# Performance work log

Measured on AMD Instinct MI355X. Metric: run time of the kernel, lower is better.

Reference implementation:

```python
import jax, jax.numpy as jnp
import numpy as np

HEADS = 8
DIM_HEAD = 64
LN_EPS = 1e-5


def rotate_half(x):
    # pairs (x0,x1) -> (-x1,x0), interleaved layout (einops '(d r)' with r=2)
    x1 = x[..., 0::2]
    x2 = x[..., 1::2]
    return jnp.stack((-x2, x1), axis=-1).reshape(x.shape)


def apply_rope(freqs, x):
    return x * jnp.cos(freqs) + rotate_half(x) * jnp.sin(freqs)


def setup_inputs() -> dict:
    key = jax.random.key(0)
    ks = jax.random.split(key, 4)
    b, n, dim = 2, 4096, 512
    inner = HEADS * DIM_HEAD
    x = jax.random.normal(ks[0], (b, n, dim), dtype=jnp.float32)
    rotary_time_emb = jax.random.uniform(ks[1], (b, n, DIM_HEAD), jnp.float32, 0.0, 6.283185)
    ln_w = jnp.ones((dim,), jnp.float32)
    ln_b = jnp.zeros((dim,), jnp.float32)
    w_qkv = jax.random.normal(ks[2], (inner * 3, dim), jnp.float32) * (dim ** -0.5)
    w_out = jax.random.normal(ks[3], (dim, inner), jnp.float32) * (inner ** -0.5)
    b_out = jnp.zeros((dim,), jnp.float32)
    return dict(x=x, rotary_time_emb=rotary_time_emb, ln_w=ln_w, ln_b=ln_b,
                w_qkv=w_qkv, w_out=w_out, b_out=b_out)


def reference(x, rotary_time_emb, ln_w, ln_b, w_qkv, w_out, b_out):
    b, n, dim = x.shape
    # LayerNorm
    mu = jnp.mean(x, axis=-1, keepdims=True)
    var = jnp.var(x, axis=-1, keepdims=True)
    xn = (x - mu) * jax.lax.rsqrt(var + LN_EPS) * ln_w + ln_b
    # QKV projection (Linear, no bias)
    qkv = xn @ w_qkv.T  # [b, n, 3*inner]
    q, k, v = jnp.split(qkv, 3, axis=-1)

    def to_heads(t):
        return t.reshape(b, n, HEADS, DIM_HEAD).transpose(0, 2, 1, 3)  # b h n d

    q, k, v = to_heads(q), to_heads(k), to_heads(v)
    freqs = rotary_time_emb[:, None, :, :]  # b 1 n d, broadcast over heads
    q = apply_rope(freqs, q)
    k = apply_rope(freqs, k)
    v = apply_rope(freqs, v)  # rotate_value=True
    scale = jnp.asarray(DIM_HEAD ** -0.5, dtype=x.dtype)
    scores = jnp.einsum('bhqd,bhkd->bhqk', q, k) * scale
    attn = jax.nn.softmax(scores, axis=-1)
    out = jnp.einsum('bhqk,bhkd->bhqd', attn, v)
    out = apply_rope(-freqs, out)  # inverse rotation of the output
    out = out.transpose(0, 2, 1, 3).reshape(b, n, HEADS * DIM_HEAD)
    return out @ w_out.T + b_out
```

## Files before the change

### kernel.cpp

```cpp
#include <hip/hip_runtime.h>
#include <cmath>

typedef short bf16x8 __attribute__((ext_vector_type(8)));
typedef float f32x2 __attribute__((ext_vector_type(2)));
typedef float f32x4 __attribute__((ext_vector_type(4)));
typedef float f32x16 __attribute__((ext_vector_type(16)));

#define NSEQ 4096
#define BATCH 2
#define DIM 512
#define HEADS 8
#define NROWS (BATCH * NSEQ)
#define QKVN (3 * DIM)

__device__ __forceinline__ unsigned short f2bf(float f) {
  unsigned int u = __float_as_uint(f);
  u += 0x7fffu + ((u >> 16) & 1u);
  return (unsigned short)(u >> 16);
}
__device__ __forceinline__ float bf2f(unsigned short h) {
  return __uint_as_float(((unsigned int)h) << 16);
}
__device__ __forceinline__ void gload16(const unsigned short* g, unsigned short* l) {
  __builtin_amdgcn_global_load_lds((const __attribute__((address_space(1))) unsigned int*)g,
                                   (__attribute__((address_space(3))) unsigned int*)l, 16, 0, 0);
}

__global__ __launch_bounds__(256) void k_prep(const float* __restrict__ rot,
                                              float* __restrict__ cosT,
                                              float* __restrict__ sinT,
                                              const float* __restrict__ wqkv,
                                              unsigned short* __restrict__ wqkb,
                                              const float* __restrict__ wout,
                                              unsigned short* __restrict__ wob,
                                              const float* __restrict__ x,
                                              const float* __restrict__ lnw,
                                              const float* __restrict__ lnb,
                                              unsigned short* __restrict__ xn) {
  const float INV2PI = 0.15915494309f;
  int bid = blockIdx.x;
  int t = threadIdx.x;
  if (bid < 2048) {
    int i = bid * 256 + t;
    float rv = rot[i] * INV2PI;
    cosT[i] = __builtin_amdgcn_cosf(rv);
    sinT[i] = __builtin_amdgcn_sinf(rv);
  } else if (bid < 5120) {
    int i = (bid - 2048) * 256 + t;
    wqkb[i] = f2bf(wqkv[i]);
  } else if (bid < 6144) {
    int i = (bid - 5120) * 256 + t;
    wob[i] = f2bf(wout[i]);
  } else {
    int row = (bid - 6144) * 4 + (t >> 6);
    int lane = t & 63;
    const float* xr = x + (size_t)row * DIM;
    float v[8];
    float s = 0.f;
#pragma unroll
    for (int j = 0; j < 8; ++j) { v[j] = xr[lane + j * 64]; s += v[j]; }
#pragma unroll
    for (int m = 1; m < 64; m <<= 1) s += __shfl_xor(s, m);
    float mu = s * (1.0f / DIM);
    float q = 0.f;
#pragma unroll
    for (int j = 0; j < 8; ++j) { float d = v[j] - mu; q += d * d; }
#pragma unroll
    for (int m = 1; m < 64; m <<= 1) q += __shfl_xor(q, m);
    float rs = rsqrtf(q * (1.0f / DIM) + 1e-5f);
#pragma unroll
    for (int j = 0; j < 8; ++j) {
      int col = lane + j * 64;
      xn[(size_t)row * DIM + col] = f2bf((v[j] - mu) * rs * lnw[col] + lnb[col]);
    }
  }
}

template <int EPI, int TM>
__global__ __launch_bounds__(256) void k_gemm(const unsigned short* __restrict__ A,
                                              const unsigned short* __restrict__ B,
                                              void* __restrict__ C,
                                              const float* __restrict__ bias,
                                              int M, int N, int K) {
  constexpr int MI = TM / 32;
  __shared__ __align__(16) unsigned short As[3][TM * 32];
  __shared__ __align__(16) unsigned short Bs[3][128 * 32];
  int bm = blockIdx.x, bn = blockIdx.y;
  int tid = threadIdx.x;
  int lane = tid & 63, w = tid >> 6;
  int wm = (w >> 1) * (TM / 2), wn = (w & 1) << 6;
  f32x4 acc[MI][4] = {};

#define GSTAGE(KT, BUF) do { \
  if constexpr (TM == 128) { \
    _Pragma("unroll") \
    for (int i = 0; i < 2; ++i) { \
      int c = tid + (i << 8); \
      int row = c >> 2, kc = (c & 3) << 3; \
      gload16(A + (size_t)(bm * 128 + row) * K + (KT) + kc, &As[BUF][(w * 64 + i * 256) * 8]); \
    } \
  } else { \
    int row = tid >> 2, kc = (tid & 3) << 3; \
    gload16(A + (size_t)(bm * 64 + row) * K + (KT) + kc, &As[BUF][(w * 64) * 8]); \
  } \
  _Pragma("unroll") \
  for (int i = 0; i < 2; ++i) { \
    int c = tid + (i << 8); \
    int row = c >> 2, kc = (c & 3) << 3; \
    gload16(B + (size_t)(bn * 128 + row) * K + (KT) + kc, &Bs[BUF][(w * 64 + i * 256) * 8]); \
  } } while (0)

  GSTAGE(0, 0);
  int nk = K >> 5;
  int rbuf = 0, wbuf = 1;
  for (int t = 0; t < nk; ++t) {
    if (t + 1 < nk) {
      GSTAGE((t + 1) << 5, wbuf);
      if constexpr (TM == 128) {
        asm volatile("s_waitcnt vmcnt(4)" ::: "memory");
      } else {
        asm volatile("s_waitcnt vmcnt(3)" ::: "memory");
      }
    } else {
      asm volatile("s_waitcnt vmcnt(0)" ::: "memory");
    }
    __builtin_amdgcn_s_barrier();
    asm volatile("" ::: "memory");
    bf16x8 af[MI], bfr[4];
#pragma unroll
    for (int mi = 0; mi < MI; ++mi)
      af[mi] = *(const bf16x8*)&As[rbuf][(wm + mi * 16 + (lane & 15)) * 32 + ((lane >> 4) << 3)];
#pragma unroll
    for (int ni = 0; ni < 4; ++ni)
      bfr[ni] = *(const bf16x8*)&Bs[rbuf][(wn + ni * 16 + (lane & 15)) * 32 + ((lane >> 4) << 3)];
#pragma unroll
    for (int mi = 0; mi < MI; ++mi)
#pragma unroll
      for (int ni = 0; ni < 4; ++ni)
        acc[mi][ni] = __builtin_amdgcn_mfma_f32_16x16x32_bf16(af[mi], bfr[ni], acc[mi][ni], 0, 0, 0);
    rbuf = (rbuf == 2) ? 0 : rbuf + 1;
    wbuf = (wbuf == 2) ? 0 : wbuf + 1;
  }
#undef GSTAGE
#pragma unroll
  for (int mi = 0; mi < MI; ++mi) {
#pragma unroll
    for (int ni = 0; ni < 4; ++ni) {
#pragma unroll
      for (int r = 0; r < 4; ++r) {
        int gm = bm * TM + wm + mi * 16 + ((lane >> 4) << 2) + r;
        int gn = bn * 128 + wn + ni * 16 + (lane & 15);
        if (EPI == 0) {
          ((unsigned short*)C)[(size_t)gm * N + gn] = f2bf(acc[mi][ni][r]);
        } else {
          ((float*)C)[(size_t)gm * N + gn] = acc[mi][ni][r] + bias[gn];
        }
      }
    }
  }
}

__global__ __launch_bounds__(256) void k_rope_split(const unsigned short* __restrict__ qkv,
                                                    const float* __restrict__ cosT,
                                                    const float* __restrict__ sinT,
                                                    unsigned short* __restrict__ qh,
                                                    unsigned short* __restrict__ kh,
                                                    unsigned short* __restrict__ vt) {
  __shared__ unsigned short vs[128][65];
  const float QSC = 0.125f * 1.44269504f;
  int nt = blockIdx.x, bh = blockIdx.y;
  int b = bh >> 3, h = bh & 7;
  int n0 = nt * 128;
  int t = threadIdx.x;
  int sub = t >> 3, cc = t & 7;
#pragma unroll
  for (int rr = 0; rr < 4; ++rr) {
    int row = rr * 32 + sub;
    int n = n0 + row;
    size_t base = ((size_t)(b * NSEQ + n)) * QKVN + h * 64 + cc * 8;
    const float* cb = cosT + ((size_t)(b * NSEQ + n)) * 64 + cc * 8;
    const float* sb = sinT + ((size_t)(b * NSEQ + n)) * 64 + cc * 8;
    float c[8], sn[8];
#pragma unroll
    for (int j = 0; j < 8; ++j) { c[j] = cb[j]; sn[j] = sb[j]; }
    bf16x8 qv = *(const bf16x8*)(qkv + base);
    bf16x8 kv = *(const bf16x8*)(qkv + base + 512);
    bf16x8 vv = *(const bf16x8*)(qkv + base + 1024);
    union { bf16x8 v; unsigned short u[8]; } yq, yk;
#pragma unroll
    for (int j = 0; j < 8; j += 2) {
      {
        float e = bf2f((unsigned short)qv[j]), o = bf2f((unsigned short)qv[j + 1]);
        yq.u[j]     = f2bf((e * c[j] - o * sn[j]) * QSC);
        yq.u[j + 1] = f2bf((o * c[j + 1] + e * sn[j + 1]) * QSC);
      }
      {
        float e = bf2f((unsigned short)kv[j]), o = bf2f((unsigned short)kv[j + 1]);
        yk.u[j]     = f2bf(e * c[j] - o * sn[j]);
        yk.u[j + 1] = f2bf(o * c[j + 1] + e * sn[j + 1]);
      }
      {
        float e = bf2f((unsigned short)vv[j]), o = bf2f((unsigned short)vv[j + 1]);
        vs[row][cc * 8 + j]     = f2bf(e * c[j] - o * sn[j]);
        vs[row][cc * 8 + j + 1] = f2bf(o * c[j + 1] + e * sn[j + 1]);
      }
    }
    *(bf16x8*)(qh + ((size_t)bh * NSEQ + n) * 64 + cc * 8) = yq.v;
    *(bf16x8*)(kh + ((size_t)bh * NSEQ + n) * 64 + cc * 8) = yk.v;
  }
  __syncthreads();
  int d = t >> 2, c4 = t & 3;
#pragma unroll
  for (int g = 0; g < 4; ++g) {
    union { bf16x8 v; unsigned short u[8]; } tv;
#pragma unroll
    for (int j = 0; j < 8; ++j) tv.u[j] = vs[c4 * 32 + g * 8 + j][d];
    *(bf16x8*)(vt + ((size_t)bh * 64 + d) * NSEQ + n0 + c4 * 32 + g * 8) = tv.v;
  }
}

__global__ __launch_bounds__(256, 2) void k_attn(const unsigned short* __restrict__ Qh,
                                                 const unsigned short* __restrict__ Kh,
                                                 const unsigned short* __restrict__ VT,
                                                 unsigned short* __restrict__ opart,
                                                 float* __restrict__ lpart) {
  __shared__ __align__(16) unsigned short Ks[4][64 * 64];
  __shared__ __align__(16) unsigned short Vs[4][64 * 64];
  int bid = blockIdx.x;
  int bh   = (bid & 7) + 8 * ((bid >> 7) & 1);
  int qt   = (bid >> 3) & 15;
  int half = (bid >> 8) & 1;
  int tid = threadIdx.x;
  int w = tid >> 6, lane = tid & 63;
  int lq = lane & 31, hi = lane >> 5;
  int q0 = qt * 256 + w * 64;
  int kv0 = half * 2048;

  const unsigned short* Kbh = Kh + (size_t)bh * NSEQ * 64;
  const unsigned short* Vbh = VT + (size_t)bh * 64 * NSEQ;

  const unsigned short* QbA = Qh + ((size_t)bh * NSEQ + q0 + lq) * 64 + hi * 8;
  const unsigned short* QbB = QbA + 32 * 64;
  bf16x8 qfA[4], qfB[4];
#pragma unroll
  for (int j = 0; j < 4; ++j) {
    qfA[j] = *(const bf16x8*)(QbA + j * 16);
    qfB[j] = *(const bf16x8*)(QbB + j * 16);
  }

  int c0 = w * 64 + lane;
  int r0 = c0 >> 3, sw0 = ((c0 & 7) ^ (r0 & 7)) << 3;
  int c1 = c0 + 256;
  int r1 = c1 >> 3, sw1 = ((c1 & 7) ^ (r1 & 7)) << 3;
  int ld0 = (w * 64) * 8, ld1 = (256 + w * 64) * 8;

  f32x16 accA0 = (f32x16)0.0f, accA1 = (f32x16)0.0f;
  f32x16 accB0 = (f32x16)0.0f, accB1 = (f32x16)0.0f;
  float lA = 0.f, lB = 0.f;
  int swz = (lq & 7) << 4;

#define STAGE(T, BUF) do { \
  int tg_ = kv0 + (T) * 64; \
  gload16(Kbh + ((size_t)tg_ + r0) * 64 + sw0, &Ks[BUF][ld0]); \
  gload16(Kbh + ((size_t)tg_ + r1) * 64 + sw1, &Ks[BUF][ld1]); \
  gload16(Vbh + (size_t)r0 * NSEQ + tg_ + sw0, &Vs[BUF][ld0]); \
  gload16(Vbh + (size_t)r1 * NSEQ + tg_ + sw1, &Vs[BUF][ld1]); \
} while (0)

  STAGE(0, 0);
  STAGE(1, 1);

  for (int t = 0; t < 32; ++t) {
    int rd = t & 3;
    if (t < 30) {
      STAGE(t + 2, (t + 2) & 3);
      asm volatile("s_waitcnt vmcnt(8)" ::: "memory");
    } else if (t == 30) {
      asm volatile("s_waitcnt vmcnt(4)" ::: "memory");
    } else {
      asm volatile("s_waitcnt vmcnt(0)" ::: "memory");
    }
    __builtin_amdgcn_s_barrier();
    asm volatile("" ::: "memory");
    const char* kb_ = (const char*)&Ks[rd][0];
    const char* vb_ = (const char*)&Vs[rd][0];
#pragma unroll
    for (int ph = 0; ph < 2; ++ph) {
      f32x16 sA = (f32x16)0.0f, sB = (f32x16)0.0f;
      __builtin_amdgcn_s_setprio(1);
#pragma unroll
      for (int j = 0; j < 4; ++j) {
        int cb = j * 32 + hi * 16;
        bf16x8 a = *(const bf16x8*)(kb_ + (ph * 32 + lq) * 128 + (cb ^ swz));
        sA = __builtin_amdgcn_mfma_f32_32x32x16_bf16(a, qfA[j], sA, 0, 0, 0);
        sB = __builtin_amdgcn_mfma_f32_32x32x16_bf16(a, qfB[j], sB, 0, 0, 0);
      }
      __builtin_amdgcn_s_setprio(0);
#pragma unroll
      for (int r = 0; r < 16; ++r) sA[r] = __builtin_amdgcn_exp2f(sA[r]);
#pragma unroll
      for (int r = 0; r < 16; ++r) sB[r] = __builtin_amdgcn_exp2f(sB[r]);
      {
        union { f32x16 v; f32x2 p[8]; } ua, ub; ua.v = sA; ub.v = sB;
        f32x2 a01 = ua.p[0] + ua.p[1], a23 = ua.p[2] + ua.p[3];
        f32x2 a45 = ua.p[4] + ua.p[5], a67 = ua.p[6] + ua.p[7];
        f32x2 ta = (a01 + a23) + (a45 + a67);
        lA += ta.x + ta.y;
        f32x2 b01 = ub.p[0] + ub.p[1], b23 = ub.p[2] + ub.p[3];
        f32x2 b45 = ub.p[4] + ub.p[5], b67 = ub.p[6] + ub.p[7];
        f32x2 tb = (b01 + b23) + (b45 + b67);
        lB += tb.x + tb.y;
      }
      unsigned int dwA[8], dwB[8];
#pragma unroll
      for (int m = 0; m < 8; ++m) {
        asm("v_cvt_pk_bf16_f32 %0, %1, %2" : "=v"(dwA[m]) : "v"(sA[2 * m]), "v"(sA[2 * m + 1]));
        asm("v_cvt_pk_bf16_f32 %0, %1, %2" : "=v"(dwB[m]) : "v"(sB[2 * m]), "v"(sB[2 * m + 1]));
      }
      __builtin_amdgcn_s_setprio(1);
#pragma unroll
      for (int kk = 0; kk < 2; ++kk) {
        const int B = 4 * kk;
        unsigned int svA0 = hi ? dwA[B + 0] : dwA[B + 2];
        unsigned int svA1 = hi ? dwA[B + 1] : dwA[B + 3];
        unsigned int svB0 = hi ? dwB[B + 0] : dwB[B + 2];
        unsigned int svB1 = hi ? dwB[B + 1] : dwB[B + 3];
        unsigned int rvA0 = (unsigned int)__shfl_xor((int)svA0, 32);
        unsigned int rvA1 = (unsigned int)__shfl_xor((int)svA1, 32);
        unsigned int rvB0 = (unsigned int)__shfl_xor((int)svB0, 32);
        unsigned int rvB1 = (unsigned int)__shfl_xor((int)svB1, 32);
        union { unsigned int d[4]; bf16x8 v; } puA, puB;
        puA.d[0] = hi ? rvA0 : dwA[B + 0];
        puA.d[1] = hi ? rvA1 : dwA[B + 1];
        puA.d[2] = hi ? dwA[B + 2] : rvA0;
        puA.d[3] = hi ? dwA[B + 3] : rvA1;
        puB.d[0] = hi ? rvB0 : dwB[B + 0];
        puB.d[1] = hi ? rvB1 : dwB[B + 1];
        puB.d[2] = hi ? dwB[B + 2] : rvB0;
        puB.d[3] = hi ? dwB[B + 3] : rvB1;
        int cb = (ph * 2 + kk) * 32 + hi * 16;
        bf16x8 v0 = *(const bf16x8*)(vb_ + lq * 128 + (cb ^ swz));
        bf16x8 v1 = *(const bf16x8*)(vb_ + (32 + lq) * 128 + (cb ^ swz));
        accA0 = __builtin_amdgcn_mfma_f32_32x32x16_bf16(v0, puA.v, accA0, 0, 0, 0);
        accA1 = __builtin_amdgcn_mfma_f32_32x32x16_bf16(v1, puA.v, accA1, 0, 0, 0);
        accB0 = __builtin_amdgcn_mfma_f32_32x32x16_bf16(v0, puB.v, accB0, 0, 0, 0);
        accB1 = __builtin_amdgcn_mfma_f32_32x32x16_bf16(v1, puB.v, accB1, 0, 0, 0);
      }
      __builtin_amdgcn_s_setprio(0);
    }
  }
#undef STAGE

  float lsumA = lA + __shfl_xor(lA, 32);
  float lsumB = lB + __shfl_xor(lB, 32);
  size_t qrowA = (size_t)(half * 16 + bh) * NSEQ + q0 + lq;
  size_t qrowB = qrowA + 32;
  if (hi == 0) {
    lpart[qrowA] = lsumA;
    lpart[qrowB] = lsumB;
  }
  unsigned short* obA = opart + qrowA * 64;
  unsigned short* obB = opart + qrowB * 64;
#pragma unroll
  for (int rg = 0; rg < 4; ++rg) {
    unsigned int pa0[2], pa1[2], pb0[2], pb1[2];
    asm("v_cvt_pk_bf16_f32 %0, %1, %2" : "=v"(pa0[0]) : "v"(accA0[4 * rg + 0]), "v"(accA0[4 * rg + 1]));
    asm("v_cvt_pk_bf16_f32 %0, %1, %2" : "=v"(pa0[1]) : "v"(accA0[4 * rg + 2]), "v"(accA0[4 * rg + 3]));
    asm("v_cvt_pk_bf16_f32 %0, %1, %2" : "=v"(pa1[0]) : "v"(accA1[4 * rg + 0]), "v"(accA1[4 * rg + 1]));
    asm("v_cvt_pk_bf16_f32 %0, %1, %2" : "=v"(pa1[1]) : "v"(accA1[4 * rg + 2]), "v"(accA1[4 * rg + 3]));
    asm("v_cvt_pk_bf16_f32 %0, %1, %2" : "=v"(pb0[0]) : "v"(accB0[4 * rg + 0]), "v"(accB0[4 * rg + 1]));
    asm("v_cvt_pk_bf16_f32 %0, %1, %2" : "=v"(pb0[1]) : "v"(accB0[4 * rg + 2]), "v"(accB0[4 * rg + 3]));
    asm("v_cvt_pk_bf16_f32 %0, %1, %2" : "=v"(pb1[0]) : "v"(accB1[4 * rg + 0]), "v"(accB1[4 * rg + 1]));
    asm("v_cvt_pk_bf16_f32 %0, %1, %2" : "=v"(pb1[1]) : "v"(accB1[4 * rg + 2]), "v"(accB1[4 * rg + 3]));
    *(uint2*)(obA + 8 * rg + 4 * hi) = *(uint2*)pa0;
    *(uint2*)(obA + 32 + 8 * rg + 4 * hi) = *(uint2*)pa1;
    *(uint2*)(obB + 8 * rg + 4 * hi) = *(uint2*)pb0;
    *(uint2*)(obB + 32 + 8 * rg + 4 * hi) = *(uint2*)pb1;
  }
}

__global__ __launch_bounds__(256) void k_combine(const unsigned short* __restrict__ opart,
                                                 const float* __restrict__ lpart,
                                                 const float* __restrict__ cosT,
                                                 const float* __restrict__ sinT,
                                                 unsigned short* __restrict__ ao) {
  int bh = blockIdx.y;
  int b = bh >> 3, h = bh & 7;
  int t = threadIdx.x;
  int q = blockIdx.x * 16 + (t >> 4);
  int d = (t & 15) * 4;
  size_t i0 = (size_t)bh * NSEQ + q;
  const size_t HOFF = (size_t)16 * NSEQ;
  float l = lpart[i0] + lpart[i0 + HOFF];
  float o[4] = {0.f, 0.f, 0.f, 0.f};
#pragma unroll
  for (int p = 0; p < 2; ++p) {
    uint2 u = *(const uint2*)(opart + (i0 + p * HOFF) * 64 + d);
    o[0] += bf2f((unsigned short)(u.x & 0xffff));
    o[1] += bf2f((unsigned short)(u.x >> 16));
    o[2] += bf2f((unsigned short)(u.y & 0xffff));
    o[3] += bf2f((unsigned short)(u.y >> 16));
  }
  float inv = 1.0f / l;
  float4 c4 = *(const float4*)(cosT + ((size_t)b * NSEQ + q) * 64 + d);
  float4 s4 = *(const float4*)(sinT + ((size_t)b * NSEQ + q) * 64 + d);
  float yx = o[0] * inv;
  float yy = o[1] * inv;
  float yz = o[2] * inv;
  float yw = o[3] * inv;
  float r0 = yx * c4.x + yy * s4.x;
  float r1 = yy * c4.y - yx * s4.y;
  float r2 = yz * c4.z + yw * s4.z;
  float r3 = yw * c4.w - yz * s4.w;
  unsigned int w0, w1;
  asm("v_cvt_pk_bf16_f32 %0, %1, %2" : "=v"(w0) : "v"(r0), "v"(r1));
  asm("v_cvt_pk_bf16_f32 %0, %1, %2" : "=v"(w1) : "v"(r2), "v"(r3));
  unsigned int uu[2] = {w0, w1};
  *(uint2*)(ao + ((size_t)b * NSEQ + q) * DIM + h * 64 + d) = *(uint2*)uu;
}

extern "C" void kernel_launch(void* const* d_in, const int* in_sizes, int n_in,
                              void* d_out, int out_size, void* d_ws, size_t ws_size,
                              hipStream_t stream) {
  const float* x    = (const float*)d_in[0];
  const float* rot  = (const float*)d_in[1];
  const float* lnw  = (const float*)d_in[2];
  const float* lnb  = (const float*)d_in[3];
  const float* wqkv = (const float*)d_in[4];
  const float* wout = (const float*)d_in[5];
  const float* bout = (const float*)d_in[6];
  float* out = (float*)d_out;

  char* ws = (char*)d_ws;
  const size_t MB = (size_t)1 << 20;
  float* cosT          = (float*)(ws + 0 * MB);
  float* sinT          = (float*)(ws + 2 * MB);
  unsigned short* wqkb = (unsigned short*)(ws + 4 * MB);
  float* lpart         = (float*)(ws + 5 * MB + 512 * 1024);
  unsigned short* wob  = (unsigned short*)(ws + 6 * MB);
  unsigned short* xn   = (unsigned short*)(ws + 8 * MB);
  unsigned short* opart = (unsigned short*)(ws + 8 * MB);
  unsigned short* qkv  = (unsigned short*)(ws + 16 * MB);
  unsigned short* qh   = (unsigned short*)(ws + 40 * MB);
  unsigned short* ao   = (unsigned short*)(ws + 40 * MB);
  unsigned short* kh   = (unsigned short*)(ws + 48 * MB);
  unsigned short* vt   = (unsigned short*)(ws + 56 * MB);

  k_prep<<<8192, 256, 0, stream>>>(rot, cosT, sinT, wqkv, wqkb, wout, wob,
                                   x, lnw, lnb, xn);
  k_gemm<0, 128><<<dim3(NROWS / 128, QKVN / 128), 256, 0, stream>>>(xn, wqkb, qkv, nullptr,
                                                                    NROWS, QKVN, DIM);
  k_rope_split<<<dim3(NSEQ / 128, 16), 256, 0, stream>>>(qkv, cosT, sinT, qh, kh, vt);
  k_attn<<<512, 256, 0, stream>>>(qh, kh, vt, opart, lpart);
  k_combine<<<dim3(NSEQ / 16, 16), 256, 0, stream>>>(opart, lpart, cosT, sinT, ao);
  k_gemm<1, 64><<<dim3(NROWS / 64, DIM / 128), 256, 0, stream>>>(ao, wob, out, bout,
                                                                 NROWS, DIM, DIM);
}
```

Baseline: 134.3 us.

## Fuse split-KV combine and inverse RoPE into output projection GEMM A-loading

Removes the separate combine kernel. The output-projection GEMM now builds its A tile directly by summing the two split-KV partial outputs, normalising by the summed softmax denominators, applying the inverse rotary rotation and packing to bf16 in LDS. This drops one launch and the write and re-read of the intermediate attention output. In exchange, each of the 4 N-blocks recomputes the combine for its rows, and the A stage now uses synchronous register loads plus ALU work inside the pipelined loop instead of async global-to-LDS loads.

```diff
diff --git a/kernel.cpp b/kernel.cpp
--- a/kernel.cpp
+++ b/kernel.cpp
@@ -76,33 +76,125 @@
   }
 }
 
-template <int EPI, int TM>
 __global__ __launch_bounds__(256) void k_gemm(const unsigned short* __restrict__ A,
                                               const unsigned short* __restrict__ B,
-                                              void* __restrict__ C,
-                                              const float* __restrict__ bias,
+                                              unsigned short* __restrict__ C,
                                               int M, int N, int K) {
-  constexpr int MI = TM / 32;
-  __shared__ __align__(16) unsigned short As[3][TM * 32];
+  __shared__ __align__(16) unsigned short As[3][128 * 32];
   __shared__ __align__(16) unsigned short Bs[3][128 * 32];
   int bm = blockIdx.x, bn = blockIdx.y;
   int tid = threadIdx.x;
   int lane = tid & 63, w = tid >> 6;
-  int wm = (w >> 1) * (TM / 2), wn = (w & 1) << 6;
-  f32x4 acc[MI][4] = {};
+  int wm = (w >> 1) << 6, wn = (w & 1) << 6;
+  f32x4 acc[4][4] = {};
 
 #define GSTAGE(KT, BUF) do { \
-  if constexpr (TM == 128) { \
-    _Pragma("unroll") \
-    for (int i = 0; i < 2; ++i) { \
-      int c = tid + (i << 8); \
-      int row = c >> 2, kc = (c & 3) << 3; \
-      gload16(A + (size_t)(bm * 128 + row) * K + (KT) + kc, &As[BUF][(w * 64 + i * 256) * 8]); \
-    } \
-  } else { \
-    int row = tid >> 2, kc = (tid & 3) << 3; \
-    gload16(A + (size_t)(bm * 64 + row) * K + (KT) + kc, &As[BUF][(w * 64) * 8]); \
-  } \
+  _Pragma("unroll") \
+  for (int i = 0; i < 2; ++i) { \
+    int c = tid + (i << 8); \
+    int row = c >> 2, kc = (c & 3) << 3; \
+    gload16(A + (size_t)(bm * 128 + row) * K + (KT) + kc, &As[BUF][(w * 64 + i * 256) * 8]); \
+    gload16(B + (size_t)(bn * 128 + row) * K + (KT) + kc, &Bs[BUF][(w * 64 + i * 256) * 8]); \
+  } } while (0)
+
+  GSTAGE(0, 0);
+  int nk = K >> 5;
+  int rbuf = 0, wbuf = 1;
+  for (int t = 0; t < nk; ++t) {
+    if (t + 1 < nk) {
+      GSTAGE((t + 1) << 5, wbuf);
+      asm volatile("s_waitcnt vmcnt(4)" ::: "memory");
+    } else {
+      asm volatile("s_waitcnt vmcnt(0)" ::: "memory");
+    }
+    __builtin_amdgcn_s_barrier();
+    asm volatile("" ::: "memory");
+    bf16x8 af[4], bfr[4];
+#pragma unroll
+    for (int mi = 0; mi < 4; ++mi)
+      af[mi] = *(const bf16x8*)&As[rbuf][(wm + mi * 16 + (lane & 15)) * 32 + ((lane >> 4) << 3)];
+#pragma unroll
+    for (int ni = 0; ni < 4; ++ni)
+      bfr[ni] = *(const bf16x8*)&Bs[rbuf][(wn + ni * 16 + (lane & 15)) * 32 + ((lane >> 4) << 3)];
+#pragma unroll
+    for (int mi = 0; mi < 4; ++mi)
+#pragma unroll
+      for (int ni = 0; ni < 4; ++ni)
+        acc[mi][ni] = __builtin_amdgcn_mfma_f32_16x16x32_bf16(af[mi], bfr[ni], acc[mi][ni], 0, 0, 0);
+    rbuf = (rbuf == 2) ? 0 : rbuf + 1;
+    wbuf = (wbuf == 2) ? 0 : wbuf + 1;
+  }
+#undef GSTAGE
+#pragma unroll
+  for (int mi = 0; mi < 4; ++mi) {
+#pragma unroll
+    for (int ni = 0; ni < 4; ++ni) {
+#pragma unroll
+      for (int r = 0; r < 4; ++r) {
+        int gm = bm * 128 + wm + mi * 16 + ((lane >> 4) << 2) + r;
+        int gn = bn * 128 + wn + ni * 16 + (lane & 15);
+        C[(size_t)gm * N + gn] = f2bf(acc[mi][ni][r]);
+      }
+    }
+  }
+}
+
+__global__ __launch_bounds__(256) void k_gemm_out(const unsigned short* __restrict__ opart,
+                                                  const float* __restrict__ lpart,
+                                                  const float* __restrict__ cosT,
+                                                  const float* __restrict__ sinT,
+                                                  const unsigned short* __restrict__ B,
+                                                  float* __restrict__ C,
+                                                  const float* __restrict__ bias) {
+  const int K = DIM, N = DIM;
+  const size_t HOFF = (size_t)16 * NSEQ;
+  __shared__ __align__(16) unsigned short As[3][64 * 32];
+  __shared__ __align__(16) unsigned short Bs[3][128 * 32];
+  int bm = blockIdx.x, bn = blockIdx.y;
+  int tid = threadIdx.x;
+  int lane = tid & 63, w = tid >> 6;
+  int wm = (w >> 1) << 5, wn = (w & 1) << 6;
+  f32x4 acc[2][4] = {};
+
+  int arow = tid >> 2, akc = (tid & 3) << 3;
+  int grow = bm * 64 + arow;
+  int b = grow >> 12, q = grow & (NSEQ - 1);
+  const float* cbase = cosT + ((size_t)b * NSEQ + q) * 64;
+  const float* sbase = sinT + ((size_t)b * NSEQ + q) * 64;
+
+#define ASTAGE(KT, BUF) do { \
+  int gc = (KT) + akc; \
+  int h = gc >> 6, d0 = gc & 63; \
+  size_t i0 = (size_t)(b * 8 + h) * NSEQ + q; \
+  float l = lpart[i0] + lpart[i0 + HOFF]; \
+  float inv = 1.0f / l; \
+  uint4 u0 = *(const uint4*)(opart + i0 * 64 + d0); \
+  uint4 u1 = *(const uint4*)(opart + (i0 + HOFF) * 64 + d0); \
+  float4 cA = *(const float4*)(cbase + d0); \
+  float4 cB = *(const float4*)(cbase + d0 + 4); \
+  float4 sA = *(const float4*)(sbase + d0); \
+  float4 sB = *(const float4*)(sbase + d0 + 4); \
+  float o0 = (bf2f((unsigned short)(u0.x & 0xffff)) + bf2f((unsigned short)(u1.x & 0xffff))) * inv; \
+  float o1 = (bf2f((unsigned short)(u0.x >> 16))    + bf2f((unsigned short)(u1.x >> 16)))    * inv; \
+  float o2 = (bf2f((unsigned short)(u0.y & 0xffff)) + bf2f((unsigned short)(u1.y & 0xffff))) * inv; \
+  float o3 = (bf2f((unsigned short)(u0.y >> 16))    + bf2f((unsigned short)(u1.y >> 16)))    * inv; \
+  float o4 = (bf2f((unsigned short)(u0.z & 0xffff)) + bf2f((unsigned short)(u1.z & 0xffff))) * inv; \
+  float o5 = (bf2f((unsigned short)(u0.z >> 16))    + bf2f((unsigned short)(u1.z >> 16)))    * inv; \
+  float o6 = (bf2f((unsigned short)(u0.w & 0xffff)) + bf2f((unsigned short)(u1.w & 0xffff))) * inv; \
+  float o7 = (bf2f((unsigned short)(u0.w >> 16))    + bf2f((unsigned short)(u1.w >> 16)))    * inv; \
+  union { unsigned short u[8]; bf16x8 v; } y; \
+  y.u[0] = f2bf(o0 * cA.x + o1 * sA.x); \
+  y.u[1] = f2bf(o1 * cA.y - o0 * sA.y); \
+  y.u[2] = f2bf(o2 * cA.z + o3 * sA.z); \
+  y.u[3] = f2bf(o3 * cA.w - o2 * sA.w); \
+  y.u[4] = f2bf(o4 * cB.x + o5 * sB.x); \
+  y.u[5] = f2bf(o5 * cB.y - o4 * sB.y); \
+  y.u[6] = f2bf(o6 * cB.z + o7 * sB.z); \
+  y.u[7] = f2bf(o7 * cB.w - o6 * sB.w); \
+  *(bf16x8*)&As[BUF][tid * 8] = y.v; \
+} while (0)
+
+#define BSTAGE(KT, BUF) do { \
   _Pragma("unroll") \
   for (int i = 0; i < 2; ++i) { \
     int c = tid + (i << 8); \
@@ -110,51 +202,46 @@
     gload16(B + (size_t)(bn * 128 + row) * K + (KT) + kc, &Bs[BUF][(w * 64 + i * 256) * 8]); \
   } } while (0)
 
-  GSTAGE(0, 0);
-  int nk = K >> 5;
+  BSTAGE(0, 0);
+  ASTAGE(0, 0);
+  const int nk = K >> 5;
   int rbuf = 0, wbuf = 1;
   for (int t = 0; t < nk; ++t) {
     if (t + 1 < nk) {
-      GSTAGE((t + 1) << 5, wbuf);
-      if constexpr (TM == 128) {
-        asm volatile("s_waitcnt vmcnt(4)" ::: "memory");
-      } else {
-        asm volatile("s_waitcnt vmcnt(3)" ::: "memory");
-      }
+      BSTAGE((t + 1) << 5, wbuf);
+      ASTAGE((t + 1) << 5, wbuf);
+      asm volatile("s_waitcnt vmcnt(2) lgkmcnt(0)" ::: "memory");
     } else {
-      asm volatile("s_waitcnt vmcnt(0)" ::: "memory");
+      asm volatile("s_waitcnt vmcnt(0) lgkmcnt(0)" ::: "memory");
     }
     __builtin_amdgcn_s_barrier();
     asm volatile("" ::: "memory");
-    bf16x8 af[MI], bfr[4];
-#pragma unroll
-    for (int mi = 0; mi < MI; ++mi)
+    bf16x8 af[2], bfr[4];
+#pragma unroll
+    for (int mi = 0; mi < 2; ++mi)
       af[mi] = *(const bf16x8*)&As[rbuf][(wm + mi * 16 + (lane & 15)) * 32 + ((lane >> 4) << 3)];
 #pragma unroll
     for (int ni = 0; ni < 4; ++ni)
       bfr[ni] = *(const bf16x8*)&Bs[rbuf][(wn + ni * 16 + (lane & 15)) * 32 + ((lane >> 4) << 3)];
 #pragma unroll
-    for (int mi = 0; mi < MI; ++mi)
+    for (int mi = 0; mi < 2; ++mi)
 #pragma unroll
       for (int ni = 0; ni < 4; ++ni)
         acc[mi][ni] = __builtin_amdgcn_mfma_f32_16x16x32_bf16(af[mi], bfr[ni], acc[mi][ni], 0, 0, 0);
     rbuf = (rbuf == 2) ? 0 : rbuf + 1;
     wbuf = (wbuf == 2) ? 0 : wbuf + 1;
   }
-#undef GSTAGE
-#pragma unroll
-  for (int mi = 0; mi < MI; ++mi) {
+#undef ASTAGE
+#undef BSTAGE
+#pragma unroll
+  for (int mi = 0; mi < 2; ++mi) {
 #pragma unroll
     for (int ni = 0; ni < 4; ++ni) {
 #pragma unroll
       for (int r = 0; r < 4; ++r) {
-        int gm = bm * TM + wm + mi * 16 + ((lane >> 4) << 2) + r;
+        int gm = bm * 64 + wm + mi * 16 + ((lane >> 4) << 2) + r;
         int gn = bn * 128 + wn + ni * 16 + (lane & 15);
-        if (EPI == 0) {
-          ((unsigned short*)C)[(size_t)gm * N + gn] = f2bf(acc[mi][ni][r]);
-        } else {
-          ((float*)C)[(size_t)gm * N + gn] = acc[mi][ni][r] + bias[gn];
-        }
+        C[(size_t)gm * N + gn] = acc[mi][ni][r] + bias[gn];
       }
     }
   }
@@ -379,46 +466,6 @@
   }
 }
 
-__global__ __launch_bounds__(256) void k_combine(const unsigned short* __restrict__ opart,
-                                                 const float* __restrict__ lpart,
-                                                 const float* __restrict__ cosT,
-                                                 const float* __restrict__ sinT,
-                                                 unsigned short* __restrict__ ao) {
-  int bh = blockIdx.y;
-  int b = bh >> 3, h = bh & 7;
-  int t = threadIdx.x;
-  int q = blockIdx.x * 16 + (t >> 4);
-  int d = (t & 15) * 4;
-  size_t i0 = (size_t)bh * NSEQ + q;
-  const size_t HOFF = (size_t)16 * NSEQ;
-  float l = lpart[i0] + lpart[i0 + HOFF];
-  float o[4] = {0.f, 0.f, 0.f, 0.f};
-#pragma unroll
-  for (int p = 0; p < 2; ++p) {
-    uint2 u = *(const uint2*)(opart + (i0 + p * HOFF) * 64 + d);
-    o[0] += bf2f((unsigned short)(u.x & 0xffff));
-    o[1] += bf2f((unsigned short)(u.x >> 16));
-    o[2] += bf2f((unsigned short)(u.y & 0xffff));
-    o[3] += bf2f((unsigned short)(u.y >> 16));
-  }
-  float inv = 1.0f / l;
-  float4 c4 = *(const float4*)(cosT + ((size_t)b * NSEQ + q) * 64 + d);
-  float4 s4 = *(const float4*)(sinT + ((size_t)b * NSEQ + q) * 64 + d);
-  float yx = o[0] * inv;
-  float yy = o[1] * inv;
-  float yz = o[2] * inv;
-  float yw = o[3] * inv;
-  float r0 = yx * c4.x + yy * s4.x;
-  float r1 = yy * c4.y - yx * s4.y;
-  float r2 = yz * c4.z + yw * s4.z;
-  float r3 = yw * c4.w - yz * s4.w;
-  unsigned int w0, w1;
-  asm("v_cvt_pk_bf16_f32 %0, %1, %2" : "=v"(w0) : "v"(r0), "v"(r1));
-  asm("v_cvt_pk_bf16_f32 %0, %1, %2" : "=v"(w1) : "v"(r2), "v"(r3));
-  unsigned int uu[2] = {w0, w1};
-  *(uint2*)(ao + ((size_t)b * NSEQ + q) * DIM + h * 64 + d) = *(uint2*)uu;
-}
-
 extern "C" void kernel_launch(void* const* d_in, const int* in_sizes, int n_in,
                               void* d_out, int out_size, void* d_ws, size_t ws_size,
                               hipStream_t stream) {
@@ -442,17 +489,15 @@
   unsigned short* opart = (unsigned short*)(ws + 8 * MB);
   unsigned short* qkv  = (unsigned short*)(ws + 16 * MB);
   unsigned short* qh   = (unsigned short*)(ws + 40 * MB);
-  unsigned short* ao   = (unsigned short*)(ws + 40 * MB);
   unsigned short* kh   = (unsigned short*)(ws + 48 * MB);
   unsigned short* vt   = (unsigned short*)(ws + 56 * MB);
 
   k_prep<<<8192, 256, 0, stream>>>(rot, cosT, sinT, wqkv, wqkb, wout, wob,
                                    x, lnw, lnb, xn);
-  k_gemm<0, 128><<<dim3(NROWS / 128, QKVN / 128), 256, 0, stream>>>(xn, wqkb, qkv, nullptr,
-                                                                    NROWS, QKVN, DIM);
+  k_gemm<<<dim3(NROWS / 128, QKVN / 128), 256, 0, stream>>>(xn, wqkb, qkv,
+                                                            NROWS, QKVN, DIM);
   k_rope_split<<<dim3(NSEQ / 128, 16), 256, 0, stream>>>(qkv, cosT, sinT, qh, kh, vt);
   k_attn<<<512, 256, 0, stream>>>(qh, kh, vt, opart, lpart);
-  k_combine<<<dim3(NSEQ / 16, 16), 256, 0, stream>>>(opart, lpart, cosT, sinT, ao);
-  k_gemm<1, 64><<<dim3(NROWS / 64, DIM / 128), 256, 0, stream>>>(ao, wob, out, bout,
-                                                                 NROWS, DIM, DIM);
-}
+  k_gemm_out<<<dim3(NROWS / 64, DIM / 128), 256, 0, stream>>>(opart, lpart, cosT, sinT,
+                                                              wob, out, bout);
+}
```

Measured after the change: 138.5 us. 3.1% more time.
